# Performance work log

Hardware: AMD Instinct MI355X
Metric: run time of the kernel (lower is better)

Reference implementation:

```python
import jax, jax.numpy as jnp
import numpy as np

N_NODES = 50000
N_EDGES = 600000
D_IN = 128
D_OUT = 128
P_DROP = 0.1
BN_EPS = 1e-5


def setup_inputs() -> dict:
    key = jax.random.key(0)
    ks = jax.random.split(key, 6)
    x = jax.random.normal(ks[0], (N_NODES, D_IN), dtype=jnp.float32)
    weight = jax.random.normal(ks[1], (D_IN, D_OUT), dtype=jnp.float32) * (1.0 / np.sqrt(D_IN))
    bias = jnp.zeros((D_OUT,), dtype=jnp.float32)
    gamma = jnp.ones((D_OUT,), dtype=jnp.float32)
    beta = jnp.zeros((D_OUT,), dtype=jnp.float32)
    dropout_u = jax.random.uniform(ks[2], (N_NODES, D_OUT), dtype=jnp.float32)
    edge_index = jax.random.randint(ks[3], (2, N_EDGES), 0, N_NODES, dtype=jnp.int64)
    return {"x": x, "weight": weight, "bias": bias, "gamma": gamma,
            "beta": beta, "dropout_u": dropout_u, "edge_index": edge_index}


def reference(x, weight, bias, gamma, beta, dropout_u, edge_index):
    N = x.shape[0]
    # --- GCNConv (add_self_loops=True, symmetric normalization) ---
    loop = jnp.arange(N, dtype=edge_index.dtype)
    src = jnp.concatenate([edge_index[0], loop])  # [E+N]
    dst = jnp.concatenate([edge_index[1], loop])  # [E+N]
    xw = x @ weight                               # [N, D_OUT] small GEMM
    deg = jnp.zeros((N,), dtype=xw.dtype).at[dst].add(1.0)
    dinv = jnp.where(deg > 0, jax.lax.rsqrt(jnp.maximum(deg, 1.0)), 0.0)
    norm = dinv[src] * dinv[dst]                  # [E+N]
    msgs = xw[src] * norm[:, None]                # gather: [E+N, D_OUT]
    z = jax.ops.segment_sum(msgs, dst, num_segments=N) + bias
    # --- activation -> BatchNorm (training stats) -> dropout ---
    z = jax.nn.relu(z)
    mean = jnp.mean(z, axis=0)
    var = jnp.mean((z - mean) ** 2, axis=0)       # biased var, as BN uses
    z = (z - mean) * jax.lax.rsqrt(var + BN_EPS) * gamma + beta
    keep = (dropout_u > P_DROP).astype(z.dtype)
    z = z * keep * (1.0 / (1.0 - P_DROP))
    return z.astype(x.dtype)
```

## Files before the change

### kernel.cpp

```cpp
#include <hip/hip_runtime.h>
#include <cstdint>
#include <cstddef>

#define D 128
#define P_DROP 0.1f
#define INV_KEEP (1.0f / 0.9f)
#define BN_EPS 1e-5f

typedef __attribute__((ext_vector_type(8))) short bf16x8;
typedef __attribute__((ext_vector_type(4))) float f32x4;

__device__ __forceinline__ unsigned f2bf(float f) {
    unsigned u = __float_as_uint(f);
    return (u + 0x7fffu + ((u >> 16) & 1u)) >> 16;
}
__device__ __forceinline__ float bf_lo(unsigned v) { return __uint_as_float(v << 16); }
__device__ __forceinline__ float bf_hi(unsigned v) { return __uint_as_float(v & 0xffff0000u); }

__global__ void k_init(float4* __restrict__ y4, int n4,
                       int* __restrict__ hist, int N,
                       float* __restrict__ bnacc,
                       int* __restrict__ ssrc, int* __restrict__ sdst, int E) {
    int stride = gridDim.x * blockDim.x;
    int i0 = blockIdx.x * blockDim.x + threadIdx.x;
    float4 z = make_float4(0.f, 0.f, 0.f, 0.f);
    for (int i = i0; i < n4; i += stride) y4[i] = z;
    for (int i = i0; i < N; i += stride) hist[i] = 0;
    if (i0 < 256) bnacc[i0] = 0.f;
    if (i0 < 64) { ssrc[E + i0] = 0; sdst[E + i0] = -1; }
}

__global__ void k_hist(const int* __restrict__ dst, int* __restrict__ hist, int E) {
    int i = blockIdx.x * blockDim.x + threadIdx.x;
    if (i < E) atomicAdd(&hist[dst[i]], 1);
}

__global__ void k_scanA(const int* __restrict__ hist, int* __restrict__ tmp,
                        int* __restrict__ blocksum, int N) {
    __shared__ int sd[256];
    int tid = threadIdx.x;
    int i = blockIdx.x * 256 + tid;
    sd[tid] = (i < N) ? hist[i] : 0;
    __syncthreads();
    for (int o = 1; o < 256; o <<= 1) {
        int t = (tid >= o) ? sd[tid - o] : 0;
        __syncthreads();
        sd[tid] += t;
        __syncthreads();
    }
    tmp[i] = sd[tid];
    if (tid == 255) blocksum[blockIdx.x] = sd[255];
}

__global__ void k_scanB(const int* __restrict__ blocksum, int* __restrict__ blockoff,
                        int NBLK) {
    __shared__ int sd[256];
    int tid = threadIdx.x;
    int v = (tid < NBLK) ? blocksum[tid] : 0;
    sd[tid] = v;
    __syncthreads();
    for (int o = 1; o < 256; o <<= 1) {
        int t = (tid >= o) ? sd[tid - o] : 0;
        __syncthreads();
        sd[tid] += t;
        __syncthreads();
    }
    if (tid < NBLK) blockoff[tid] = sd[tid] - v;
}

__global__ void k_scanC(const int* __restrict__ tmp, const int* __restrict__ blockoff,
                        const int* __restrict__ hist, int* __restrict__ cursor, int N) {
    int i = blockIdx.x * 256 + threadIdx.x;
    if (i < N) cursor[i] = tmp[i] + blockoff[blockIdx.x] - hist[i];
}

__global__ void k_place(const int* __restrict__ src, const int* __restrict__ dst,
                        int* __restrict__ cursor,
                        int* __restrict__ ssrc, int* __restrict__ sdst, int E) {
    int i = blockIdx.x * blockDim.x + threadIdx.x;
    if (i < E) {
        int d = dst[i];
        int p = atomicAdd(&cursor[d], 1);
        ssrc[p] = src[i];
        sdst[p] = d;
    }
}

__global__ __launch_bounds__(256) void k_gemm(
    const float* __restrict__ x, const float* __restrict__ w,
    const int* __restrict__ hist, unsigned short* __restrict__ xwb,
    float* __restrict__ dinv, int N) {
    __shared__ unsigned short xs[64][136];
    __shared__ unsigned short wt[128][136];
    int tid = threadIdx.x;
    int row0 = blockIdx.x * 64;

#pragma unroll
    for (int i = 0; i < 32; ++i) {
        int flat = tid + i * 256;
        int n = flat & 127;
        int kp = flat >> 7;
        float a0 = w[(size_t)(2 * kp) * D + n];
        float a1 = w[(size_t)(2 * kp + 1) * D + n];
        *(unsigned*)&wt[n][2 * kp] = f2bf(a0) | (f2bf(a1) << 16);
    }
#pragma unroll
    for (int i = 0; i < 8; ++i) {
        int flat = tid + i * 256;
        int r = flat >> 5;
        int kq = flat & 31;
        int row = row0 + r;
        float4 v = (row < N) ? *(const float4*)&x[(size_t)row * D + kq * 4]
                             : make_float4(0.f, 0.f, 0.f, 0.f);
        uint2 pk;
        pk.x = f2bf(v.x) | (f2bf(v.y) << 16);
        pk.y = f2bf(v.z) | (f2bf(v.w) << 16);
        *(uint2*)&xs[r][kq * 4] = pk;
    }
    __syncthreads();

    int wv = tid >> 6, lane = tid & 63;
    int l15 = lane & 15, quad = lane >> 4;
    int mrow = wv * 16 + l15;
    f32x4 acc[8];
#pragma unroll
    for (int t = 0; t < 8; ++t) acc[t] = (f32x4){0.f, 0.f, 0.f, 0.f};
#pragma unroll
    for (int k0 = 0; k0 < D; k0 += 32) {
        bf16x8 af = *(bf16x8*)&xs[mrow][k0 + quad * 8];
#pragma unroll
        for (int nt = 0; nt < 8; ++nt) {
            bf16x8 bfr = *(bf16x8*)&wt[nt * 16 + l15][k0 + quad * 8];
            acc[nt] = __builtin_amdgcn_mfma_f32_16x16x32_bf16(af, bfr, acc[nt], 0, 0, 0);
        }
    }
#pragma unroll
    for (int reg = 0; reg < 4; ++reg) {
        int node = row0 + wv * 16 + quad * 4 + reg;
        if (node < N) {
            float dv = rsqrtf((float)(hist[node] + 1));
            if (l15 == 0) dinv[node] = dv;
#pragma unroll
            for (int nt = 0; nt < 8; ++nt) {
                float val = acc[nt][reg] * dv;
                xwb[(size_t)node * D + nt * 16 + l15] = (unsigned short)f2bf(val);
            }
        }
    }
}

__global__ __launch_bounds__(256) void k_aggregate(
    const unsigned short* __restrict__ xwb, const float* __restrict__ dinv,
    const int* __restrict__ ssrc, const int* __restrict__ sdst,
    float* __restrict__ y, int E) {
    int lane = threadIdx.x & 63;
    int wv = threadIdx.x >> 6;
    int w = blockIdx.x * 4 + wv;
    int e0 = w * 64;
    if (e0 >= E) return;

    int vsrc = ssrc[e0 + lane];
    int vdst = sdst[e0 + lane];
    int prevd = (w > 0) ? __builtin_amdgcn_readfirstlane(sdst[e0 - 1]) : -5;
    int nextd = __builtin_amdgcn_readfirstlane(sdst[e0 + 64]);
    int cidx = vdst < 0 ? 0 : vdst;
    float dvv = dinv[cidx];

    float a0 = 0.f, a1 = 0.f;
    int cur = __builtin_amdgcn_readlane(vdst, 0);
    bool excl = (prevd != cur);

    unsigned vrow[32];
#pragma unroll
    for (int half = 0; half < 2; ++half) {
        int base = half * 32;
#pragma unroll
        for (int j = 0; j < 32; ++j) {
            int idx = __builtin_amdgcn_readlane(vsrc, base + j);
            vrow[j] = *(const unsigned*)(xwb + (size_t)idx * D + lane * 2);
        }
#pragma unroll
        for (int j = 0; j < 32; ++j) {
            int gj = base + j;
            int dj = __builtin_amdgcn_readlane(vdst, gj);
            if (dj != cur) {
                float dv = __int_as_float(
                    __builtin_amdgcn_readlane(__float_as_int(dvv), gj - 1));
                float s0 = a0 * dv, s1 = a1 * dv;
                float* yp = y + (size_t)cur * D + lane * 2;
                if (excl) { *(float2*)yp = make_float2(s0, s1); }
                else { atomicAdd(yp, s0); atomicAdd(yp + 1, s1); }
                a0 = 0.f; a1 = 0.f; cur = dj; excl = true;
            }
            unsigned v = vrow[j];
            a0 += bf_lo(v); a1 += bf_hi(v);
        }
    }
    if (cur >= 0) {
        float dv = __int_as_float(__builtin_amdgcn_readlane(__float_as_int(dvv), 63));
        float s0 = a0 * dv, s1 = a1 * dv;
        float* yp = y + (size_t)cur * D + lane * 2;
        if (excl && (nextd != cur)) { *(float2*)yp = make_float2(s0, s1); }
        else { atomicAdd(yp, s0); atomicAdd(yp + 1, s1); }
    }
}

__global__ __launch_bounds__(256) void k_postagg(
    float* __restrict__ y, const unsigned short* __restrict__ xwb,
    const float* __restrict__ dinv, const float* __restrict__ bias,
    float* __restrict__ bnacc, int total4) {
    int tid = threadIdx.x;
    int stride = gridDim.x * 256;
    int c4 = tid & 31;
    float4 b4 = ((const float4*)bias)[c4];
    float s0 = 0.f, s1 = 0.f, s2 = 0.f, s3 = 0.f;
    float q0 = 0.f, q1 = 0.f, q2 = 0.f, q3 = 0.f;
    for (int i = blockIdx.x * 256 + tid; i < total4; i += stride) {
        int node = i >> 5;
        float4 z = ((float4*)y)[i];
        uint2 sv = *(const uint2*)(xwb + (size_t)node * D + c4 * 4);
        float dv = dinv[node];
        z.x = fmaxf(fmaf(bf_lo(sv.x), dv, z.x) + b4.x, 0.f);
        z.y = fmaxf(fmaf(bf_hi(sv.x), dv, z.y) + b4.y, 0.f);
        z.z = fmaxf(fmaf(bf_lo(sv.y), dv, z.z) + b4.z, 0.f);
        z.w = fmaxf(fmaf(bf_hi(sv.y), dv, z.w) + b4.w, 0.f);
        ((float4*)y)[i] = z;
        s0 += z.x; s1 += z.y; s2 += z.z; s3 += z.w;
        q0 += z.x * z.x; q1 += z.y * z.y; q2 += z.z * z.z; q3 += z.w * z.w;
    }
    __shared__ float red[256][8];
    red[tid][0] = s0; red[tid][1] = s1; red[tid][2] = s2; red[tid][3] = s3;
    red[tid][4] = q0; red[tid][5] = q1; red[tid][6] = q2; red[tid][7] = q3;
    __syncthreads();
    if (tid < 128) {
        int r0 = tid >> 2, sl = tid & 3;
        float acc = 0.f;
#pragma unroll
        for (int m = 0; m < 8; ++m) acc += red[r0 + 32 * m][sl];
        atomicAdd(&bnacc[tid], acc);
    } else {
        int t = tid - 128;
        int r0 = t >> 2, sl = 4 + (t & 3);
        float acc = 0.f;
#pragma unroll
        for (int m = 0; m < 8; ++m) acc += red[r0 + 32 * m][sl];
        atomicAdd(&bnacc[128 + t], acc);
    }
}

__global__ void k_bnfinal(const float* __restrict__ bnacc, const float* __restrict__ gamma,
                          const float* __restrict__ beta, float* __restrict__ scsh, int N) {
    int c = threadIdx.x;
    if (c < 128) {
        float invN = 1.0f / (float)N;
        float mean = bnacc[c] * invN;
        float var = bnacc[128 + c] * invN - mean * mean;
        var = fmaxf(var, 0.f);
        float sc = gamma[c] * rsqrtf(var + BN_EPS);
        scsh[c] = sc;
        scsh[128 + c] = beta[c] - mean * sc;
    }
}

__global__ __launch_bounds__(256) void k_finalize(
    float* __restrict__ out, const float* __restrict__ u,
    const float* __restrict__ scsh, int total4) {
    int i = blockIdx.x * 256 + threadIdx.x;
    if (i >= total4) return;
    float4 v = ((const float4*)out)[i];
    float4 uu = ((const float4*)u)[i];
    int c = (i & 31) * 4;
    float s0 = scsh[c], s1 = scsh[c + 1], s2 = scsh[c + 2], s3 = scsh[c + 3];
    float h0 = scsh[128 + c], h1 = scsh[128 + c + 1];
    float h2 = scsh[128 + c + 2], h3 = scsh[128 + c + 3];
    v.x = fmaf(v.x, s0, h0) * (uu.x > P_DROP ? INV_KEEP : 0.f);
    v.y = fmaf(v.y, s1, h1) * (uu.y > P_DROP ? INV_KEEP : 0.f);
    v.z = fmaf(v.z, s2, h2) * (uu.z > P_DROP ? INV_KEEP : 0.f);
    v.w = fmaf(v.w, s3, h3) * (uu.w > P_DROP ? INV_KEEP : 0.f);
    ((float4*)out)[i] = v;
}

extern "C" void kernel_launch(void* const* d_in, const int* in_sizes, int n_in,
                              void* d_out, int out_size, void* d_ws, size_t ws_size,
                              hipStream_t stream) {
    const float* x      = (const float*)d_in[0];
    const float* weight = (const float*)d_in[1];
    const float* bias   = (const float*)d_in[2];
    const float* gamma  = (const float*)d_in[3];
    const float* beta   = (const float*)d_in[4];
    const float* du     = (const float*)d_in[5];
    const int*   eidx   = (const int*)d_in[6];
    float* out = (float*)d_out;

    const int N = in_sizes[0] / D;
    const int E = in_sizes[6] / 2;
    const int* esrc = eidx;
    const int* edst = eidx + E;

    char* p = (char*)d_ws;
    auto alloc = [&](size_t bytes) {
        char* q = p;
        p += (bytes + 255) & ~(size_t)255;
        return q;
    };
    unsigned short* xwb = (unsigned short*)alloc((size_t)N * D * sizeof(unsigned short));
    int*   hist     = (int*)alloc((size_t)N * sizeof(int));
    int*   cursor   = (int*)alloc((size_t)N * sizeof(int));
    const int NBLK = (N + 255) / 256;
    int*   tmp      = (int*)alloc((size_t)NBLK * 256 * sizeof(int));
    int*   blocksum = (int*)alloc((size_t)NBLK * sizeof(int));
    int*   blockoff = (int*)alloc((size_t)NBLK * sizeof(int));
    int*   ssrc     = (int*)alloc((size_t)(E + 64) * sizeof(int));
    int*   sdst     = (int*)alloc((size_t)(E + 64) * sizeof(int));
    float* dinv     = (float*)alloc((size_t)N * sizeof(float));
    float* bnacc    = (float*)alloc(256 * sizeof(float));
    float* scsh     = (float*)alloc(256 * sizeof(float));

    const int EB = (E + 255) / 256;
    const int total4 = N * (D / 4);
    hipLaunchKernelGGL(k_init, dim3(1024), dim3(256), 0, stream,
                       (float4*)out, total4, hist, N, bnacc, ssrc, sdst, E);
    hipLaunchKernelGGL(k_hist, dim3(EB), dim3(256), 0, stream, edst, hist, E);
    hipLaunchKernelGGL(k_scanA, dim3(NBLK), dim3(256), 0, stream, hist, tmp, blocksum, N);
    hipLaunchKernelGGL(k_scanB, dim3(1), dim3(256), 0, stream, blocksum, blockoff, NBLK);
    hipLaunchKernelGGL(k_scanC, dim3(NBLK), dim3(256), 0, stream, tmp, blockoff, hist, cursor, N);
    hipLaunchKernelGGL(k_place, dim3(EB), dim3(256), 0, stream, esrc, edst, cursor, ssrc, sdst, E);
    hipLaunchKernelGGL(k_gemm, dim3((N + 63) / 64), dim3(256), 0, stream,
                       x, weight, hist, xwb, dinv, N);
    const int NWAVE = (E + 63) / 64;
    hipLaunchKernelGGL(k_aggregate, dim3((NWAVE + 3) / 4), dim3(256), 0, stream,
                       xwb, dinv, ssrc, sdst, out, E);
    hipLaunchKernelGGL(k_postagg, dim3(1024), dim3(256), 0, stream,
                       out, xwb, dinv, bias, bnacc, total4);
    hipLaunchKernelGGL(k_bnfinal, dim3(1), dim3(128), 0, stream, bnacc, gamma, beta, scsh, N);
    hipLaunchKernelGGL(k_finalize, dim3((total4 + 255) / 256), dim3(256), 0, stream,
                       out, du, scsh, total4);
}
```

Before: 257.4 us.

## Merge scan stages, fold self-loops into CSR, make stats pass read-only

Replaces the three-kernel scan with a single 1024-thread block scan that also writes dinv, and fuses zero-init into the histogram kernel using a memset. Self-loops now go into the sorted edge list as extra entries, so the post-aggregation pass no longer gathers xwb and no longer rewrites y. The BN stats pass only reads y, and the final kernel recomputes bias+ReLU and folds the BN scale/shift computation into itself. This cuts kernel launches and one full read-write of the output. The cost is a serial single-block scan over 50k nodes and recomputing bias+ReLU in the final pass.

```diff
diff --git a/kernel.cpp b/kernel.cpp
--- a/kernel.cpp
+++ b/kernel.cpp
@@ -16,90 +16,76 @@
 }
 __device__ __forceinline__ float bf_lo(unsigned v) { return __uint_as_float(v << 16); }
 __device__ __forceinline__ float bf_hi(unsigned v) { return __uint_as_float(v & 0xffff0000u); }
-
-__global__ void k_init(float4* __restrict__ y4, int n4,
-                       int* __restrict__ hist, int N,
-                       float* __restrict__ bnacc,
-                       int* __restrict__ ssrc, int* __restrict__ sdst, int E) {
-    int stride = gridDim.x * blockDim.x;
-    int i0 = blockIdx.x * blockDim.x + threadIdx.x;
+__device__ __forceinline__ float rl_f(float v, int l) {
+    return __int_as_float(__builtin_amdgcn_readlane(__float_as_int(v), l));
+}
+
+__global__ __launch_bounds__(256) void k_hist(
+    const int* __restrict__ edst, int* __restrict__ hist, int E,
+    float4* __restrict__ y4, int total4) {
+    int gt = blockIdx.x * 256 + threadIdx.x;
+    int stride = gridDim.x * 256;
     float4 z = make_float4(0.f, 0.f, 0.f, 0.f);
-    for (int i = i0; i < n4; i += stride) y4[i] = z;
-    for (int i = i0; i < N; i += stride) hist[i] = 0;
-    if (i0 < 256) bnacc[i0] = 0.f;
-    if (i0 < 64) { ssrc[E + i0] = 0; sdst[E + i0] = -1; }
-}
-
-__global__ void k_hist(const int* __restrict__ dst, int* __restrict__ hist, int E) {
-    int i = blockIdx.x * blockDim.x + threadIdx.x;
-    if (i < E) atomicAdd(&hist[dst[i]], 1);
-}
-
-__global__ void k_scanA(const int* __restrict__ hist, int* __restrict__ tmp,
-                        int* __restrict__ blocksum, int N) {
-    __shared__ int sd[256];
+    for (int i = gt; i < total4; i += stride) y4[i] = z;
+    for (int i = gt; i < E; i += stride) atomicAdd(&hist[edst[i]], 1);
+}
+
+__global__ __launch_bounds__(1024) void k_scan(
+    const int* __restrict__ hist, int* __restrict__ cursor,
+    float* __restrict__ dinv, int N) {
+    __shared__ int wsum[16];
+    __shared__ int carry;
     int tid = threadIdx.x;
-    int i = blockIdx.x * 256 + tid;
-    sd[tid] = (i < N) ? hist[i] : 0;
+    int lane = tid & 63, wv = tid >> 6;
+    if (tid == 0) carry = 0;
     __syncthreads();
-    for (int o = 1; o < 256; o <<= 1) {
-        int t = (tid >= o) ? sd[tid - o] : 0;
+    const int NC = (N + 1023) >> 10;
+    int dnext = (tid < N) ? hist[tid] + 1 : 0;
+    for (int c = 0; c < NC; ++c) {
+        int d = dnext;
+        int inext = (c + 1) * 1024 + tid;
+        if (c + 1 < NC) dnext = (inext < N) ? hist[inext] + 1 : 0;
+        int base = carry;
+        int s = d;
+#pragma unroll
+        for (int off = 1; off < 64; off <<= 1) {
+            int t = __shfl_up(s, off, 64);
+            if (lane >= off) s += t;
+        }
+        if (lane == 63) wsum[wv] = s;
         __syncthreads();
-        sd[tid] += t;
+        if (wv == 0 && lane < 16) {
+            int v = wsum[lane];
+#pragma unroll
+            for (int off = 1; off < 16; off <<= 1) {
+                int t = __shfl_up(v, off, 64);
+                if (lane >= off) v += t;
+            }
+            wsum[lane] = v;
+        }
         __syncthreads();
-    }
-    tmp[i] = sd[tid];
-    if (tid == 255) blocksum[blockIdx.x] = sd[255];
-}
-
-__global__ void k_scanB(const int* __restrict__ blocksum, int* __restrict__ blockoff,
-                        int NBLK) {
-    __shared__ int sd[256];
-    int tid = threadIdx.x;
-    int v = (tid < NBLK) ? blocksum[tid] : 0;
-    sd[tid] = v;
-    __syncthreads();
-    for (int o = 1; o < 256; o <<= 1) {
-        int t = (tid >= o) ? sd[tid - o] : 0;
+        int prefix = base + (wv ? wsum[wv - 1] : 0);
+        int i = c * 1024 + tid;
+        if (i < N) {
+            cursor[i] = prefix + s - d;
+            dinv[i] = rsqrtf((float)d);
+        }
+        if (tid == 0) carry = base + wsum[15];
         __syncthreads();
-        sd[tid] += t;
-        __syncthreads();
-    }
-    if (tid < NBLK) blockoff[tid] = sd[tid] - v;
-}
-
-__global__ void k_scanC(const int* __restrict__ tmp, const int* __restrict__ blockoff,
-                        const int* __restrict__ hist, int* __restrict__ cursor, int N) {
-    int i = blockIdx.x * 256 + threadIdx.x;
-    if (i < N) cursor[i] = tmp[i] + blockoff[blockIdx.x] - hist[i];
-}
-
-__global__ void k_place(const int* __restrict__ src, const int* __restrict__ dst,
-                        int* __restrict__ cursor,
-                        int* __restrict__ ssrc, int* __restrict__ sdst, int E) {
-    int i = blockIdx.x * blockDim.x + threadIdx.x;
-    if (i < E) {
-        int d = dst[i];
-        int p = atomicAdd(&cursor[d], 1);
-        ssrc[p] = src[i];
-        sdst[p] = d;
     }
 }
 
 __global__ __launch_bounds__(256) void k_gemm(
     const float* __restrict__ x, const float* __restrict__ w,
-    const int* __restrict__ hist, unsigned short* __restrict__ xwb,
-    float* __restrict__ dinv, int N) {
+    const float* __restrict__ dinv, unsigned short* __restrict__ xwb, int N) {
     __shared__ unsigned short xs[64][136];
     __shared__ unsigned short wt[128][136];
     int tid = threadIdx.x;
     int row0 = blockIdx.x * 64;
-
 #pragma unroll
     for (int i = 0; i < 32; ++i) {
         int flat = tid + i * 256;
-        int n = flat & 127;
-        int kp = flat >> 7;
+        int n = flat & 127, kp = flat >> 7;
         float a0 = w[(size_t)(2 * kp) * D + n];
         float a1 = w[(size_t)(2 * kp + 1) * D + n];
         *(unsigned*)&wt[n][2 * kp] = f2bf(a0) | (f2bf(a1) << 16);
@@ -107,8 +93,7 @@
 #pragma unroll
     for (int i = 0; i < 8; ++i) {
         int flat = tid + i * 256;
-        int r = flat >> 5;
-        int kq = flat & 31;
+        int r = flat >> 5, kq = flat & 31;
         int row = row0 + r;
         float4 v = (row < N) ? *(const float4*)&x[(size_t)row * D + kq * 4]
                              : make_float4(0.f, 0.f, 0.f, 0.f);
@@ -118,13 +103,12 @@
         *(uint2*)&xs[r][kq * 4] = pk;
     }
     __syncthreads();
-
     int wv = tid >> 6, lane = tid & 63;
     int l15 = lane & 15, quad = lane >> 4;
     int mrow = wv * 16 + l15;
     f32x4 acc[8];
 #pragma unroll
-    for (int t = 0; t < 8; ++t) acc[t] = (f32x4){0.f, 0.f, 0.f, 0.f};
+    for (int a = 0; a < 8; ++a) acc[a] = (f32x4){0.f, 0.f, 0.f, 0.f};
 #pragma unroll
     for (int k0 = 0; k0 < D; k0 += 32) {
         bf16x8 af = *(bf16x8*)&xs[mrow][k0 + quad * 8];
@@ -138,8 +122,7 @@
     for (int reg = 0; reg < 4; ++reg) {
         int node = row0 + wv * 16 + quad * 4 + reg;
         if (node < N) {
-            float dv = rsqrtf((float)(hist[node] + 1));
-            if (l15 == 0) dinv[node] = dv;
+            float dv = dinv[node];
 #pragma unroll
             for (int nt = 0; nt < 8; ++nt) {
                 float val = acc[nt][reg] * dv;
@@ -149,27 +132,43 @@
     }
 }
 
-__global__ __launch_bounds__(256) void k_aggregate(
+__global__ __launch_bounds__(256) void k_place(
+    const int* __restrict__ esrc, const int* __restrict__ edst,
+    int* __restrict__ cursor, int* __restrict__ ssrc, int* __restrict__ sdst,
+    int E, int N) {
+    int gt = blockIdx.x * 256 + threadIdx.x;
+    int stride = gridDim.x * 256;
+    if (gt < 64) { ssrc[E + N + gt] = 0; sdst[E + N + gt] = -1; }
+    for (int i = gt; i < E; i += stride) {
+        int d = edst[i];
+        int q = atomicAdd(&cursor[d], 1);
+        ssrc[q] = esrc[i];
+        sdst[q] = d;
+    }
+    for (int n = gt; n < N; n += stride) {
+        int q = atomicAdd(&cursor[n], 1);
+        ssrc[q] = n;
+        sdst[q] = n;
+    }
+}
+
+__global__ __launch_bounds__(256) void k_agg(
     const unsigned short* __restrict__ xwb, const float* __restrict__ dinv,
     const int* __restrict__ ssrc, const int* __restrict__ sdst,
-    float* __restrict__ y, int E) {
+    float* __restrict__ y, int NTASK) {
     int lane = threadIdx.x & 63;
     int wv = threadIdx.x >> 6;
     int w = blockIdx.x * 4 + wv;
+    if (w >= NTASK) return;
     int e0 = w * 64;
-    if (e0 >= E) return;
-
     int vsrc = ssrc[e0 + lane];
     int vdst = sdst[e0 + lane];
     int prevd = (w > 0) ? __builtin_amdgcn_readfirstlane(sdst[e0 - 1]) : -5;
     int nextd = __builtin_amdgcn_readfirstlane(sdst[e0 + 64]);
-    int cidx = vdst < 0 ? 0 : vdst;
-    float dvv = dinv[cidx];
-
+    float dvv = dinv[vdst < 0 ? 0 : vdst];
     float a0 = 0.f, a1 = 0.f;
     int cur = __builtin_amdgcn_readlane(vdst, 0);
     bool excl = (prevd != cur);
-
     unsigned vrow[32];
 #pragma unroll
     for (int half = 0; half < 2; ++half) {
@@ -184,8 +183,7 @@
             int gj = base + j;
             int dj = __builtin_amdgcn_readlane(vdst, gj);
             if (dj != cur) {
-                float dv = __int_as_float(
-                    __builtin_amdgcn_readlane(__float_as_int(dvv), gj - 1));
+                float dv = rl_f(dvv, gj - 1);
                 float s0 = a0 * dv, s1 = a1 * dv;
                 float* yp = y + (size_t)cur * D + lane * 2;
                 if (excl) { *(float2*)yp = make_float2(s0, s1); }
@@ -197,7 +195,7 @@
         }
     }
     if (cur >= 0) {
-        float dv = __int_as_float(__builtin_amdgcn_readlane(__float_as_int(dvv), 63));
+        float dv = rl_f(dvv, 63);
         float s0 = a0 * dv, s1 = a1 * dv;
         float* yp = y + (size_t)cur * D + lane * 2;
         if (excl && (nextd != cur)) { *(float2*)yp = make_float2(s0, s1); }
@@ -205,26 +203,22 @@
     }
 }
 
-__global__ __launch_bounds__(256) void k_postagg(
-    float* __restrict__ y, const unsigned short* __restrict__ xwb,
-    const float* __restrict__ dinv, const float* __restrict__ bias,
+__global__ __launch_bounds__(256) void k_stats(
+    const float* __restrict__ y, const float* __restrict__ bias,
     float* __restrict__ bnacc, int total4) {
     int tid = threadIdx.x;
-    int stride = gridDim.x * 256;
-    int c4 = tid & 31;
+    int gt = blockIdx.x * 256 + tid;
+    int gstride = gridDim.x * 256;
+    int c4 = gt & 31;
     float4 b4 = ((const float4*)bias)[c4];
     float s0 = 0.f, s1 = 0.f, s2 = 0.f, s3 = 0.f;
     float q0 = 0.f, q1 = 0.f, q2 = 0.f, q3 = 0.f;
-    for (int i = blockIdx.x * 256 + tid; i < total4; i += stride) {
-        int node = i >> 5;
-        float4 z = ((float4*)y)[i];
-        uint2 sv = *(const uint2*)(xwb + (size_t)node * D + c4 * 4);
-        float dv = dinv[node];
-        z.x = fmaxf(fmaf(bf_lo(sv.x), dv, z.x) + b4.x, 0.f);
-        z.y = fmaxf(fmaf(bf_hi(sv.x), dv, z.y) + b4.y, 0.f);
-        z.z = fmaxf(fmaf(bf_lo(sv.y), dv, z.z) + b4.z, 0.f);
-        z.w = fmaxf(fmaf(bf_hi(sv.y), dv, z.w) + b4.w, 0.f);
-        ((float4*)y)[i] = z;
+    for (int i = gt; i < total4; i += gstride) {
+        float4 z = ((const float4*)y)[i];
+        z.x = fmaxf(z.x + b4.x, 0.f);
+        z.y = fmaxf(z.y + b4.y, 0.f);
+        z.z = fmaxf(z.z + b4.z, 0.f);
+        z.w = fmaxf(z.w + b4.w, 0.f);
         s0 += z.x; s1 += z.y; s2 += z.z; s3 += z.w;
         q0 += z.x * z.x; q1 += z.y * z.y; q2 += z.z * z.z; q3 += z.w * z.w;
     }
@@ -239,45 +233,52 @@
         for (int m = 0; m < 8; ++m) acc += red[r0 + 32 * m][sl];
         atomicAdd(&bnacc[tid], acc);
     } else {
-        int t = tid - 128;
-        int r0 = t >> 2, sl = 4 + (t & 3);
+        int t2 = tid - 128;
+        int r0 = t2 >> 2, sl = 4 + (t2 & 3);
         float acc = 0.f;
 #pragma unroll
         for (int m = 0; m < 8; ++m) acc += red[r0 + 32 * m][sl];
-        atomicAdd(&bnacc[128 + t], acc);
-    }
-}
-
-__global__ void k_bnfinal(const float* __restrict__ bnacc, const float* __restrict__ gamma,
-                          const float* __restrict__ beta, float* __restrict__ scsh, int N) {
-    int c = threadIdx.x;
-    if (c < 128) {
+        atomicAdd(&bnacc[128 + t2], acc);
+    }
+}
+
+__global__ __launch_bounds__(256) void k_final(
+    float* __restrict__ y, const float* __restrict__ du,
+    const float* __restrict__ bias, const float* __restrict__ gamma,
+    const float* __restrict__ beta, const float* __restrict__ bnacc,
+    int N, int total4) {
+    __shared__ float scl[128];
+    __shared__ float shf[128];
+    int tid = threadIdx.x;
+    if (tid < 128) {
         float invN = 1.0f / (float)N;
-        float mean = bnacc[c] * invN;
-        float var = bnacc[128 + c] * invN - mean * mean;
-        var = fmaxf(var, 0.f);
-        float sc = gamma[c] * rsqrtf(var + BN_EPS);
-        scsh[c] = sc;
-        scsh[128 + c] = beta[c] - mean * sc;
-    }
-}
-
-__global__ __launch_bounds__(256) void k_finalize(
-    float* __restrict__ out, const float* __restrict__ u,
-    const float* __restrict__ scsh, int total4) {
-    int i = blockIdx.x * 256 + threadIdx.x;
-    if (i >= total4) return;
-    float4 v = ((const float4*)out)[i];
-    float4 uu = ((const float4*)u)[i];
-    int c = (i & 31) * 4;
-    float s0 = scsh[c], s1 = scsh[c + 1], s2 = scsh[c + 2], s3 = scsh[c + 3];
-    float h0 = scsh[128 + c], h1 = scsh[128 + c + 1];
-    float h2 = scsh[128 + c + 2], h3 = scsh[128 + c + 3];
-    v.x = fmaf(v.x, s0, h0) * (uu.x > P_DROP ? INV_KEEP : 0.f);
-    v.y = fmaf(v.y, s1, h1) * (uu.y > P_DROP ? INV_KEEP : 0.f);
-    v.z = fmaf(v.z, s2, h2) * (uu.z > P_DROP ? INV_KEEP : 0.f);
-    v.w = fmaf(v.w, s3, h3) * (uu.w > P_DROP ? INV_KEEP : 0.f);
-    ((float4*)out)[i] = v;
+        float mean = bnacc[tid] * invN;
+        float var = fmaxf(bnacc[128 + tid] * invN - mean * mean, 0.f);
+        float sc = gamma[tid] * rsqrtf(var + BN_EPS);
+        scl[tid] = sc;
+        shf[tid] = beta[tid] - mean * sc;
+    }
+    __syncthreads();
+    int gt = blockIdx.x * 256 + tid;
+    int gstride = gridDim.x * 256;
+    int c4 = gt & 31;
+    float4 b4 = ((const float4*)bias)[c4];
+    float sc0 = scl[c4 * 4], sc1 = scl[c4 * 4 + 1], sc2 = scl[c4 * 4 + 2], sc3 = scl[c4 * 4 + 3];
+    float sh0 = shf[c4 * 4], sh1 = shf[c4 * 4 + 1], sh2 = shf[c4 * 4 + 2], sh3 = shf[c4 * 4 + 3];
+    for (int i = gt; i < total4; i += gstride) {
+        float4 z = ((const float4*)y)[i];
+        float4 uu = ((const float4*)du)[i];
+        z.x = fmaxf(z.x + b4.x, 0.f);
+        z.y = fmaxf(z.y + b4.y, 0.f);
+        z.z = fmaxf(z.z + b4.z, 0.f);
+        z.w = fmaxf(z.w + b4.w, 0.f);
+        float4 v;
+        v.x = fmaf(z.x, sc0, sh0) * (uu.x > P_DROP ? INV_KEEP : 0.f);
+        v.y = fmaf(z.y, sc1, sh1) * (uu.y > P_DROP ? INV_KEEP : 0.f);
+        v.z = fmaf(z.z, sc2, sh2) * (uu.z > P_DROP ? INV_KEEP : 0.f);
+        v.w = fmaf(z.w, sc3, sh3) * (uu.w > P_DROP ? INV_KEEP : 0.f);
+        ((float4*)y)[i] = v;
+    }
 }
 
 extern "C" void kernel_launch(void* const* d_in, const int* in_sizes, int n_in,
@@ -294,45 +295,40 @@
 
     const int N = in_sizes[0] / D;
     const int E = in_sizes[6] / 2;
+    const int EN = E + N;
     const int* esrc = eidx;
     const int* edst = eidx + E;
 
-    char* p = (char*)d_ws;
+    char* pws = (char*)d_ws;
     auto alloc = [&](size_t bytes) {
-        char* q = p;
-        p += (bytes + 255) & ~(size_t)255;
+        char* q = pws;
+        pws += (bytes + 255) & ~(size_t)255;
         return q;
     };
     unsigned short* xwb = (unsigned short*)alloc((size_t)N * D * sizeof(unsigned short));
-    int*   hist     = (int*)alloc((size_t)N * sizeof(int));
-    int*   cursor   = (int*)alloc((size_t)N * sizeof(int));
-    const int NBLK = (N + 255) / 256;
-    int*   tmp      = (int*)alloc((size_t)NBLK * 256 * sizeof(int));
-    int*   blocksum = (int*)alloc((size_t)NBLK * sizeof(int));
-    int*   blockoff = (int*)alloc((size_t)NBLK * sizeof(int));
-    int*   ssrc     = (int*)alloc((size_t)(E + 64) * sizeof(int));
-    int*   sdst     = (int*)alloc((size_t)(E + 64) * sizeof(int));
-    float* dinv     = (float*)alloc((size_t)N * sizeof(float));
-    float* bnacc    = (float*)alloc(256 * sizeof(float));
-    float* scsh     = (float*)alloc(256 * sizeof(float));
-
-    const int EB = (E + 255) / 256;
+    int*   hist   = (int*)alloc((size_t)N * sizeof(int));
+    float* bnacc  = (float*)alloc(256 * sizeof(float));
+    int*   cursor = (int*)alloc((size_t)N * sizeof(int));
+    int*   ssrc   = (int*)alloc((size_t)(EN + 64) * sizeof(int));
+    int*   sdst   = (int*)alloc((size_t)(EN + 64) * sizeof(int));
+    float* dinv   = (float*)alloc((size_t)N * sizeof(float));
+
     const int total4 = N * (D / 4);
-    hipLaunchKernelGGL(k_init, dim3(1024), dim3(256), 0, stream,
-                       (float4*)out, total4, hist, N, bnacc, ssrc, sdst, E);
-    hipLaunchKernelGGL(k_hist, dim3(EB), dim3(256), 0, stream, edst, hist, E);
-    hipLaunchKernelGGL(k_scanA, dim3(NBLK), dim3(256), 0, stream, hist, tmp, blocksum, N);
-    hipLaunchKernelGGL(k_scanB, dim3(1), dim3(256), 0, stream, blocksum, blockoff, NBLK);
-    hipLaunchKernelGGL(k_scanC, dim3(NBLK), dim3(256), 0, stream, tmp, blockoff, hist, cursor, N);
-    hipLaunchKernelGGL(k_place, dim3(EB), dim3(256), 0, stream, esrc, edst, cursor, ssrc, sdst, E);
+    const int NTASK = (EN + 63) / 64;
+
+    size_t zspan = (size_t)((char*)(bnacc + 256) - (char*)hist);
+    hipMemsetAsync(hist, 0, zspan, stream);
+    hipLaunchKernelGGL(k_hist, dim3(1024), dim3(256), 0, stream,
+                       edst, hist, E, (float4*)out, total4);
+    hipLaunchKernelGGL(k_scan, dim3(1), dim3(1024), 0, stream, hist, cursor, dinv, N);
     hipLaunchKernelGGL(k_gemm, dim3((N + 63) / 64), dim3(256), 0, stream,
-                       x, weight, hist, xwb, dinv, N);
-    const int NWAVE = (E + 63) / 64;
-    hipLaunchKernelGGL(k_aggregate, dim3((NWAVE + 3) / 4), dim3(256), 0, stream,
-                       xwb, dinv, ssrc, sdst, out, E);
-    hipLaunchKernelGGL(k_postagg, dim3(1024), dim3(256), 0, stream,
-                       out, xwb, dinv, bias, bnacc, total4);
-    hipLaunchKernelGGL(k_bnfinal, dim3(1), dim3(128), 0, stream, bnacc, gamma, beta, scsh, N);
-    hipLaunchKernelGGL(k_finalize, dim3((total4 + 255) / 256), dim3(256), 0, stream,
-                       out, du, scsh, total4);
-}
+                       x, weight, dinv, xwb, N);
+    hipLaunchKernelGGL(k_place, dim3(1024), dim3(256), 0, stream,
+                       esrc, edst, cursor, ssrc, sdst, E, N);
+    hipLaunchKernelGGL(k_agg, dim3((NTASK + 3) / 4), dim3(256), 0, stream,
+                       xwb, dinv, ssrc, sdst, out, NTASK);
+    hipLaunchKernelGGL(k_stats, dim3(1024), dim3(256), 0, stream,
+                       out, bias, bnacc, total4);
+    hipLaunchKernelGGL(k_final, dim3(1024), dim3(256), 0, stream,
+                       out, du, bias, gamma, beta, bnacc, N, total4);
+}
```

Result: slower. 305.4 us (+18.6%).
